# Kernel tuning notes

Hardware: AMD Instinct MI355X
Metric: run time of the kernel (lower is better)

## Reference

```python
import jax, jax.numpy as jnp
import numpy as np
import math

N, LQ, C = 4, 5440, 256
H, L, P = 8, 4, 4
D = C // H
SHAPES = [(64, 64), (32, 32), (16, 16), (8, 8)]
STARTS = [0, 4096, 5120, 5376]
LEN_IN = 5440


def setup_inputs() -> dict:
    key = jax.random.key(0)
    ks = jax.random.split(key, 12)
    s = 1.0 / math.sqrt(C)
    return {
        "query": jax.random.normal(ks[0], (N, LQ, C), jnp.float32),
        "reference_points": jax.random.uniform(ks[1], (N, LQ, L, 2), jnp.float32),
        "input_flatten": jax.random.normal(ks[2], (N, LEN_IN, C), jnp.float32),
        "input_spatial_shapes": jnp.asarray(SHAPES, jnp.int32),
        "input_level_start_index": jnp.asarray(STARTS, jnp.int32),
        "w_off": jax.random.normal(ks[3], (C, H * L * P * 2), jnp.float32) * 0.01,
        "b_off": jax.random.normal(ks[4], (H * L * P * 2,), jnp.float32) * 0.5,
        "w_attn": jax.random.normal(ks[5], (C, H * L * P), jnp.float32) * 0.01,
        "b_attn": jnp.zeros((H * L * P,), jnp.float32),
        "w_val": jax.random.normal(ks[6], (C, C), jnp.float32) * s,
        "b_val": jnp.zeros((C,), jnp.float32),
        "w_out": jax.random.normal(ks[7], (C, C), jnp.float32) * s,
        "b_out": jnp.zeros((C,), jnp.float32),
    }


def _gather_corner(lv, yi, xi, w):
    # lv: (N, h*w, H, D); yi, xi: (N, Lq, H, P) int32 -> (N, Lq, H, P, D)
    n, lq, h_, p_ = yi.shape
    idx = yi * w + xi
    idx2 = idx.transpose(0, 1, 3, 2).reshape(n, lq * p_, h_)[..., None]
    g = jnp.take_along_axis(lv, idx2, axis=1)  # (N, Lq*P, H, D)
    return g.reshape(n, lq, p_, h_, -1).transpose(0, 1, 3, 2, 4)


def _msdeform(query, reference_points, input_flatten, shapes, starts,
              w_off, b_off, w_attn, b_attn, w_val, b_val, w_out, b_out):
    n, lq, c = query.shape
    value = (input_flatten @ w_val + b_val).reshape(n, -1, H, D)
    off = (query @ w_off + b_off).reshape(n, lq, H, L, P, 2)
    attn = jax.nn.softmax((query @ w_attn + b_attn).reshape(n, lq, H, L * P), axis=-1)
    # sampling locations in [0,1], (N, Lq, H, L, P, 2)
    loc = jnp.clip(reference_points[:, :, None, :, None, :] + off, 0.0, 1.0)
    sampled = []
    for lvl, (hh, ww) in enumerate(shapes):
        s0 = starts[lvl]
        lv = value[:, s0:s0 + hh * ww]  # (N, hh*ww, H, D)
        xy = loc[:, :, :, lvl] * jnp.asarray([ww, hh], jnp.float32) - 0.5  # (N,Lq,H,P,2)
        x, y = xy[..., 0], xy[..., 1]
        x0 = jnp.floor(x)
        y0 = jnp.floor(y)
        x0i = jnp.clip(x0.astype(jnp.int32), 0, ww - 1)
        x1i = jnp.clip(x0.astype(jnp.int32) + 1, 0, ww - 1)
        y0i = jnp.clip(y0.astype(jnp.int32), 0, hh - 1)
        y1i = jnp.clip(y0.astype(jnp.int32) + 1, 0, hh - 1)
        x0f, x1f = x0i.astype(x.dtype), x1i.astype(x.dtype)
        y0f, y1f = y0i.astype(y.dtype), y1i.astype(y.dtype)
        wa = ((x1f - x) * (y1f - y))[..., None]
        wb = ((x1f - x) * (y - y0f))[..., None]
        wc = ((x - x0f) * (y1f - y))[..., None]
        wd = ((x - x0f) * (y - y0f))[..., None]
        va = _gather_corner(lv, y0i, x0i, ww)
        vb = _gather_corner(lv, y1i, x0i, ww)
        vc = _gather_corner(lv, y0i, x1i, ww)
        vd = _gather_corner(lv, y1i, x1i, ww)
        sampled.append(wa * va + wb * vb + wc * vc + wd * vd)
    sampled = jnp.concatenate(sampled, axis=3)  # (N, Lq, H, L*P, D)
    out = jnp.einsum('nqhp,nqhpd->nqhd', attn, sampled).reshape(n, lq, c)
    return out @ w_out + b_out


def reference(query, reference_points, input_flatten, input_spatial_shapes,
              input_level_start_index, w_off, b_off, w_attn, b_attn,
              w_val, b_val, w_out, b_out):
    shapes = [tuple(int(v) for v in row) for row in np.asarray(input_spatial_shapes)]
    starts = [int(v) for v in np.asarray(input_level_start_index)]
    return _msdeform(query, reference_points, input_flatten, shapes, starts,
                     w_off, b_off, w_attn, b_attn, w_val, b_val, w_out, b_out)
```

## Files before the change

### kernel.cpp

```cpp
#include <hip/hip_runtime.h>
#include <hip/hip_fp16.h>
#include <math.h>

#define C_DIM 256
#define H_DIM 8
#define L_DIM 4
#define P_DIM 4
#define LQ 5440
#define LEN_IN 5440
#define NB 4
#define M_ROWS (NB * LQ)

typedef __attribute__((ext_vector_type(8))) _Float16 f16x8;
typedef __attribute__((ext_vector_type(8))) unsigned short u16x8;
typedef __attribute__((ext_vector_type(4))) float f32x4;

__device__ __forceinline__ void split_f32(float a, __half& h, __half& l) {
    h = __float2half(a);
    l = __float2half(a - __half2float(h));
}

__global__ __launch_bounds__(256) void convert_wt(const float* __restrict__ w,
                                                  __half* __restrict__ hi,
                                                  __half* __restrict__ lo, int ncols) {
    const int ncol = blockIdx.x;
    const int k = threadIdx.x;
    const float a = w[(size_t)k * ncols + ncol];
    __half h, l;
    split_f32(a, h, l);
    hi[(size_t)ncol * 256 + k] = h;
    lo[(size_t)ncol * 256 + k] = l;
}

template <int NC>
__global__ __launch_bounds__(256, 2) void gemm_f16x3(const float* __restrict__ A,
                                                     const __half* __restrict__ Bhi,
                                                     const __half* __restrict__ Blo,
                                                     const float* __restrict__ bias,
                                                     float* __restrict__ outp) {
    __shared__ __align__(16) __half sA[2][128][32];
    __shared__ __align__(16) __half sB[2][128][32];

    const int n0 = blockIdx.x * 128;
    const int row0 = blockIdx.y * 128;
    const int t = threadIdx.x;
    const int w = t >> 6, lane = t & 63;
    const int bm = (w >> 1) * 64, bn = (w & 1) * 64;
    const int fr = lane & 15;
    const int fc = lane >> 4;

    const int ar1 = t >> 2, ar2 = ar1 + 64;
    const int ak8 = t & 3;
    const int asw1 = (ak8 ^ ((ar1 >> 1) & 3)) * 8;
    const int asw2 = (ak8 ^ ((ar2 >> 1) & 3)) * 8;
    const int br1 = t >> 2, br2 = br1 + 64;
    const int bc8 = t & 3;
    const int bsw1 = (bc8 ^ ((br1 >> 1) & 3)) * 8;
    const int bsw2 = (bc8 ^ ((br2 >> 1) & 3)) * 8;

    const size_t ga1 = (size_t)(row0 + ar1) * 256 + ak8 * 8;
    const size_t ga2 = (size_t)(row0 + ar2) * 256 + ak8 * 8;
    const size_t gb1 = (size_t)(n0 + br1) * 256 + bc8 * 8;
    const size_t gb2 = (size_t)(n0 + br2) * 256 + bc8 * 8;

    f32x4 acc[4][4];
#pragma unroll
    for (int m = 0; m < 4; ++m)
#pragma unroll
        for (int n = 0; n < 4; ++n)
#pragma unroll
            for (int r = 0; r < 4; ++r) acc[m][n][r] = 0.f;

    float4 pa[4];
    float4 pb[4];
    pa[0] = *(const float4*)(A + ga1);
    pa[1] = *(const float4*)(A + ga1 + 4);
    pa[2] = *(const float4*)(A + ga2);
    pa[3] = *(const float4*)(A + ga2 + 4);
    pb[0] = *(const float4*)(Bhi + gb1);
    pb[1] = *(const float4*)(Bhi + gb2);
    pb[2] = *(const float4*)(Blo + gb1);
    pb[3] = *(const float4*)(Blo + gb2);

    for (int kt = 0; kt < 8; ++kt) {
        if (kt) __syncthreads();
#pragma unroll
        for (int ch = 0; ch < 2; ++ch) {
            const float4 u = pa[2 * ch], v = pa[2 * ch + 1];
            const float e[8] = {u.x, u.y, u.z, u.w, v.x, v.y, v.z, v.w};
            u16x8 Hh, Ll;
#pragma unroll
            for (int i = 0; i < 8; ++i) {
                __half h, l;
                split_f32(e[i], h, l);
                Hh[i] = __half_as_ushort(h);
                Ll[i] = __half_as_ushort(l);
            }
            const int row = ch ? ar2 : ar1;
            const int sw = ch ? asw2 : asw1;
            *(u16x8*)&sA[0][row][sw] = Hh;
            *(u16x8*)&sA[1][row][sw] = Ll;
        }
        *(float4*)&sB[0][br1][bsw1] = pb[0];
        *(float4*)&sB[0][br2][bsw2] = pb[1];
        *(float4*)&sB[1][br1][bsw1] = pb[2];
        *(float4*)&sB[1][br2][bsw2] = pb[3];
        __syncthreads();
        if (kt < 7) {
            const size_t ko = (size_t)(kt + 1) * 32;
            pa[0] = *(const float4*)(A + ga1 + ko);
            pa[1] = *(const float4*)(A + ga1 + ko + 4);
            pa[2] = *(const float4*)(A + ga2 + ko);
            pa[3] = *(const float4*)(A + ga2 + ko + 4);
            pb[0] = *(const float4*)(Bhi + gb1 + ko);
            pb[1] = *(const float4*)(Bhi + gb2 + ko);
            pb[2] = *(const float4*)(Blo + gb1 + ko);
            pb[3] = *(const float4*)(Blo + gb2 + ko);
        }

        f16x8 bhf[4], blf[4];
#pragma unroll
        for (int n = 0; n < 4; ++n) {
            const int rowb = bn + n * 16 + fr;
            const int swb = (fc ^ ((rowb >> 1) & 3)) * 8;
            bhf[n] = *(const f16x8*)&sB[0][rowb][swb];
            blf[n] = *(const f16x8*)&sB[1][rowb][swb];
        }
#pragma unroll
        for (int m = 0; m < 4; ++m) {
            const int rowa = bm + m * 16 + fr;
            const int swa = (fc ^ ((rowa >> 1) & 3)) * 8;
            const f16x8 ah = *(const f16x8*)&sA[0][rowa][swa];
            const f16x8 al = *(const f16x8*)&sA[1][rowa][swa];
#pragma unroll
            for (int n = 0; n < 4; ++n) {
                acc[m][n] = __builtin_amdgcn_mfma_f32_16x16x32_f16(ah, bhf[n], acc[m][n], 0, 0, 0);
                acc[m][n] = __builtin_amdgcn_mfma_f32_16x16x32_f16(al, bhf[n], acc[m][n], 0, 0, 0);
                acc[m][n] = __builtin_amdgcn_mfma_f32_16x16x32_f16(ah, blf[n], acc[m][n], 0, 0, 0);
            }
        }
    }

#pragma unroll
    for (int n = 0; n < 4; ++n) {
        const int col = n0 + bn + n * 16 + fr;
        const float bv = bias[col];
#pragma unroll
        for (int m = 0; m < 4; ++m) {
            const int row = row0 + bm + m * 16 + fc * 4;
#pragma unroll
            for (int r = 0; r < 4; ++r)
                outp[(size_t)(row + r) * NC + col] = acc[m][n][r] + bv;
        }
    }
}

__global__ __launch_bounds__(128) void sample_kernel(const float* __restrict__ value,
                                                     const float* __restrict__ ol,
                                                     const float* __restrict__ refpts,
                                                     float* __restrict__ tmp) {
    const int t = threadIdx.x;
    const int w = t >> 6, lane = t & 63;
    const int q = blockIdx.x * 2 + w;
    const int n = q / LQ;

    __shared__ __align__(16) float4 s_aw[2][128];
    __shared__ __align__(16) int4 s_of[2][128];

#pragma unroll
    for (int s = 0; s < 2; ++s) {
        const int j = lane + 64 * s;
        const int h = j >> 4, lp = j & 15;
        const int l = lp >> 2;
        const int ww = 64 >> l;
        int st = 0;
        if (l == 1) st = 4096;
        else if (l == 2) st = 5120;
        else if (l == 3) st = 5376;

        const float2 oxy = *(const float2*)&ol[(size_t)q * 384 + 2 * j];
        const float2 rxy = *(const float2*)&refpts[((size_t)q * L_DIM + l) * 2];

        const float fw = (float)ww;
        const float x = fminf(fmaxf(rxy.x + oxy.x, 0.f), 1.f) * fw - 0.5f;
        const float y = fminf(fmaxf(rxy.y + oxy.y, 0.f), 1.f) * fw - 0.5f;
        const int xi = (int)floorf(x);
        const int yi = (int)floorf(y);
        const int x0i = min(max(xi, 0), ww - 1);
        const int x1i = min(max(xi + 1, 0), ww - 1);
        const int y0i = min(max(yi, 0), ww - 1);
        const int y1i = min(max(yi + 1, 0), ww - 1);
        const float wx0 = (float)x1i - x, wx1 = x - (float)x0i;
        const float wy0 = (float)y1i - y, wy1 = y - (float)y0i;

        const float lg = ol[(size_t)q * 384 + 256 + j];
        float m = lg;
#pragma unroll
        for (int o = 8; o; o >>= 1) m = fmaxf(m, __shfl_xor(m, o, 16));
        const float e = expf(lg - m);
        float sm = e;
#pragma unroll
        for (int o = 8; o; o >>= 1) sm += __shfl_xor(sm, o, 16);
        const float a = e / sm;

        const int p = lp * 8 + (h ^ (lp & 7));
        float4 aw;
        aw.x = a * (wx0 * wy0);
        aw.y = a * (wx0 * wy1);
        aw.z = a * (wx1 * wy0);
        aw.w = a * (wx1 * wy1);
        int4 of;
        of.x = (st + y0i * ww + x0i) << 10;
        of.y = (st + y1i * ww + x0i) << 10;
        of.z = (st + y0i * ww + x1i) << 10;
        of.w = (st + y1i * ww + x1i) << 10;
        s_aw[w][p] = aw;
        s_of[w][p] = of;
    }
    __syncthreads();

    const int h = lane >> 3;
    const char* vb = (const char*)value + (size_t)n * LEN_IN * C_DIM * 4 + (size_t)(lane * 16);
    float4 acc;
    acc.x = 0.f; acc.y = 0.f; acc.z = 0.f; acc.w = 0.f;
#pragma unroll
    for (int lp = 0; lp < 16; ++lp) {
        const int p = lp * 8 + (h ^ (lp & 7));
        const float4 aw = s_aw[w][p];
        const int4 of = s_of[w][p];
        const float4 v0 = *(const float4*)(vb + of.x);
        const float4 v1 = *(const float4*)(vb + of.y);
        const float4 v2 = *(const float4*)(vb + of.z);
        const float4 v3 = *(const float4*)(vb + of.w);
        acc.x += aw.x * v0.x + aw.y * v1.x + aw.z * v2.x + aw.w * v3.x;
        acc.y += aw.x * v0.y + aw.y * v1.y + aw.z * v2.y + aw.w * v3.y;
        acc.z += aw.x * v0.z + aw.y * v1.z + aw.z * v2.z + aw.w * v3.z;
        acc.w += aw.x * v0.w + aw.y * v1.w + aw.z * v2.w + aw.w * v3.w;
    }
    *(float4*)&tmp[(size_t)q * 256 + (size_t)(lane * 4)] = acc;
}

extern "C" void kernel_launch(void* const* d_in, const int* in_sizes, int n_in,
                              void* d_out, int out_size, void* d_ws, size_t ws_size,
                              hipStream_t stream) {
    const float* query         = (const float*)d_in[0];
    const float* refpts        = (const float*)d_in[1];
    const float* input_flatten = (const float*)d_in[2];
    const float* w_off  = (const float*)d_in[5];
    const float* b_off  = (const float*)d_in[6];
    const float* w_attn = (const float*)d_in[7];
    const float* b_attn = (const float*)d_in[8];
    const float* w_val  = (const float*)d_in[9];
    const float* b_val  = (const float*)d_in[10];
    const float* w_out  = (const float*)d_in[11];
    const float* b_out  = (const float*)d_in[12];
    float* out = (float*)d_out;

    const size_t nr = (size_t)M_ROWS;
    float* p = (float*)d_ws;
    float* value_ws = p; p += nr * 256;
    float* ol_ws    = p; p += nr * 384;
    float* tmp_ws   = p; p += nr * 256;
    float* bc_ws    = p; p += 384;
    __half* wv_hi = (__half*)p;
    __half* wv_lo = wv_hi + 256 * 256;
    __half* wc_hi = wv_lo + 256 * 256;
    __half* wc_lo = wc_hi + 384 * 256;
    __half* wt_hi = wc_lo + 384 * 256;
    __half* wt_lo = wt_hi + 256 * 256;

    convert_wt<<<256, 256, 0, stream>>>(w_val, wv_hi, wv_lo, 256);
    convert_wt<<<256, 256, 0, stream>>>(w_off, wc_hi, wc_lo, 256);
    convert_wt<<<128, 256, 0, stream>>>(w_attn, wc_hi + 256 * 256, wc_lo + 256 * 256, 128);
    convert_wt<<<256, 256, 0, stream>>>(w_out, wt_hi, wt_lo, 256);
    hipMemcpyAsync(bc_ws, b_off, 256 * sizeof(float), hipMemcpyDeviceToDevice, stream);
    hipMemcpyAsync(bc_ws + 256, b_attn, 128 * sizeof(float), hipMemcpyDeviceToDevice, stream);

    dim3 g256(2, M_ROWS / 128);
    dim3 g384(3, M_ROWS / 128);

    gemm_f16x3<256><<<g256, 256, 0, stream>>>(input_flatten, wv_hi, wv_lo, b_val, value_ws);
    gemm_f16x3<384><<<g384, 256, 0, stream>>>(query, wc_hi, wc_lo, bc_ws, ol_ws);

    sample_kernel<<<M_ROWS / 2, 128, 0, stream>>>(value_ws, ol_ws, refpts, tmp_ws);

    gemm_f16x3<256><<<g256, 256, 0, stream>>>(tmp_ws, wt_hi, wt_lo, b_out, out);
}
```

Measured before the change: 154.8 us.

## Merge weight conversions, narrow GEMM N-tile, and batch queries per sample block

Four weight-conversion launches and two bias memcpys become a single convert_all kernel to cut launch overhead. The GEMM is templated on N-tile width and min-waves, and the 256-column GEMMs now use 64-wide tiles with occupancy 3, giving more blocks and more resident waves. The sampling kernel moves to 256-thread blocks, each wave handling two queries in sequence, and uses unsigned offsets for address arithmetic. Narrower N tiles make each block reload the A operand more often, and fewer sample blocks could reduce latency hiding.

Measured after the change: 142.3 us. 1.09x faster.

```diff
diff --git a/kernel.cpp b/kernel.cpp
--- a/kernel.cpp
+++ b/kernel.cpp
@@ -20,32 +20,52 @@
     l = __float2half(a - __half2float(h));
 }
 
-__global__ __launch_bounds__(256) void convert_wt(const float* __restrict__ w,
-                                                  __half* __restrict__ hi,
-                                                  __half* __restrict__ lo, int ncols) {
-    const int ncol = blockIdx.x;
-    const int k = threadIdx.x;
-    const float a = w[(size_t)k * ncols + ncol];
-    __half h, l;
-    split_f32(a, h, l);
-    hi[(size_t)ncol * 256 + k] = h;
-    lo[(size_t)ncol * 256 + k] = l;
-}
-
-template <int NC>
-__global__ __launch_bounds__(256, 2) void gemm_f16x3(const float* __restrict__ A,
-                                                     const __half* __restrict__ Bhi,
-                                                     const __half* __restrict__ Blo,
-                                                     const float* __restrict__ bias,
-                                                     float* __restrict__ outp) {
+__global__ __launch_bounds__(256) void convert_all(const float* __restrict__ w_val,
+                                                   const float* __restrict__ w_off,
+                                                   const float* __restrict__ w_attn,
+                                                   const float* __restrict__ w_out,
+                                                   const float* __restrict__ b_off,
+                                                   const float* __restrict__ b_attn,
+                                                   __half* __restrict__ wv_hi, __half* __restrict__ wv_lo,
+                                                   __half* __restrict__ wc_hi, __half* __restrict__ wc_lo,
+                                                   __half* __restrict__ wt_hi, __half* __restrict__ wt_lo,
+                                                   float* __restrict__ bc) {
+    const int b = blockIdx.x, k = threadIdx.x;
+    if (b < 896) {
+        const float* w; __half *hi, *lo; int ncols, col, orow;
+        if (b < 256)      { w = w_val;  hi = wv_hi; lo = wv_lo; ncols = 256; col = b;       orow = col; }
+        else if (b < 512) { w = w_off;  hi = wc_hi; lo = wc_lo; ncols = 256; col = b - 256; orow = col; }
+        else if (b < 640) { w = w_attn; hi = wc_hi; lo = wc_lo; ncols = 128; col = b - 512; orow = col + 256; }
+        else              { w = w_out;  hi = wt_hi; lo = wt_lo; ncols = 256; col = b - 640; orow = col; }
+        const float a = w[(size_t)k * ncols + col];
+        __half h, l;
+        split_f32(a, h, l);
+        hi[(size_t)orow * 256 + k] = h;
+        lo[(size_t)orow * 256 + k] = l;
+    } else if (b == 896) {
+        bc[k] = b_off[k];
+    } else {
+        if (k < 128) bc[256 + k] = b_attn[k];
+    }
+}
+
+template <int NC, int BN, int MINW>
+__global__ __launch_bounds__(256, MINW) void gemm_f16x3(const float* __restrict__ A,
+                                                        const __half* __restrict__ Bhi,
+                                                        const __half* __restrict__ Blo,
+                                                        const float* __restrict__ bias,
+                                                        float* __restrict__ outp) {
+    constexpr int NF = BN / 32;
+    constexpr int BCH = BN / 64;
+
     __shared__ __align__(16) __half sA[2][128][32];
-    __shared__ __align__(16) __half sB[2][128][32];
-
-    const int n0 = blockIdx.x * 128;
+    __shared__ __align__(16) __half sB[2][BN][32];
+
+    const int n0 = blockIdx.x * BN;
     const int row0 = blockIdx.y * 128;
     const int t = threadIdx.x;
     const int w = t >> 6, lane = t & 63;
-    const int bm = (w >> 1) * 64, bn = (w & 1) * 64;
+    const int bm = (w >> 1) * 64, bn = (w & 1) * (BN / 2);
     const int fr = lane & 15;
     const int fc = lane >> 4;
 
@@ -53,34 +73,39 @@
     const int ak8 = t & 3;
     const int asw1 = (ak8 ^ ((ar1 >> 1) & 3)) * 8;
     const int asw2 = (ak8 ^ ((ar2 >> 1) & 3)) * 8;
-    const int br1 = t >> 2, br2 = br1 + 64;
     const int bc8 = t & 3;
-    const int bsw1 = (bc8 ^ ((br1 >> 1) & 3)) * 8;
-    const int bsw2 = (bc8 ^ ((br2 >> 1) & 3)) * 8;
+    int brr[BCH], bsw[BCH];
+#pragma unroll
+    for (int c = 0; c < BCH; ++c) {
+        brr[c] = (t >> 2) + 64 * c;
+        bsw[c] = (bc8 ^ ((brr[c] >> 1) & 3)) * 8;
+    }
 
     const size_t ga1 = (size_t)(row0 + ar1) * 256 + ak8 * 8;
     const size_t ga2 = (size_t)(row0 + ar2) * 256 + ak8 * 8;
-    const size_t gb1 = (size_t)(n0 + br1) * 256 + bc8 * 8;
-    const size_t gb2 = (size_t)(n0 + br2) * 256 + bc8 * 8;
-
-    f32x4 acc[4][4];
+    size_t gb[BCH];
+#pragma unroll
+    for (int c = 0; c < BCH; ++c) gb[c] = (size_t)(n0 + brr[c]) * 256 + bc8 * 8;
+
+    f32x4 acc[4][NF];
 #pragma unroll
     for (int m = 0; m < 4; ++m)
 #pragma unroll
-        for (int n = 0; n < 4; ++n)
+        for (int n = 0; n < NF; ++n)
 #pragma unroll
             for (int r = 0; r < 4; ++r) acc[m][n][r] = 0.f;
 
     float4 pa[4];
-    float4 pb[4];
+    float4 pb[2 * BCH];
     pa[0] = *(const float4*)(A + ga1);
     pa[1] = *(const float4*)(A + ga1 + 4);
     pa[2] = *(const float4*)(A + ga2);
     pa[3] = *(const float4*)(A + ga2 + 4);
-    pb[0] = *(const float4*)(Bhi + gb1);
-    pb[1] = *(const float4*)(Bhi + gb2);
-    pb[2] = *(const float4*)(Blo + gb1);
-    pb[3] = *(const float4*)(Blo + gb2);
+#pragma unroll
+    for (int c = 0; c < BCH; ++c) {
+        pb[c] = *(const float4*)(Bhi + gb[c]);
+        pb[BCH + c] = *(const float4*)(Blo + gb[c]);
+    }
 
     for (int kt = 0; kt < 8; ++kt) {
         if (kt) __syncthreads();
@@ -101,10 +126,11 @@
             *(u16x8*)&sA[0][row][sw] = Hh;
             *(u16x8*)&sA[1][row][sw] = Ll;
         }
-        *(float4*)&sB[0][br1][bsw1] = pb[0];
-        *(float4*)&sB[0][br2][bsw2] = pb[1];
-        *(float4*)&sB[1][br1][bsw1] = pb[2];
-        *(float4*)&sB[1][br2][bsw2] = pb[3];
+#pragma unroll
+        for (int c = 0; c < BCH; ++c) {
+            *(float4*)&sB[0][brr[c]][bsw[c]] = pb[c];
+            *(float4*)&sB[1][brr[c]][bsw[c]] = pb[BCH + c];
+        }
         __syncthreads();
         if (kt < 7) {
             const size_t ko = (size_t)(kt + 1) * 32;
@@ -112,15 +138,16 @@
             pa[1] = *(const float4*)(A + ga1 + ko + 4);
             pa[2] = *(const float4*)(A + ga2 + ko);
             pa[3] = *(const float4*)(A + ga2 + ko + 4);
-            pb[0] = *(const float4*)(Bhi + gb1 + ko);
-            pb[1] = *(const float4*)(Bhi + gb2 + ko);
-            pb[2] = *(const float4*)(Blo + gb1 + ko);
-            pb[3] = *(const float4*)(Blo + gb2 + ko);
-        }
-
-        f16x8 bhf[4], blf[4];
-#pragma unroll
-        for (int n = 0; n < 4; ++n) {
+#pragma unroll
+            for (int c = 0; c < BCH; ++c) {
+                pb[c] = *(const float4*)(Bhi + gb[c] + ko);
+                pb[BCH + c] = *(const float4*)(Blo + gb[c] + ko);
+            }
+        }
+
+        f16x8 bhf[NF], blf[NF];
+#pragma unroll
+        for (int n = 0; n < NF; ++n) {
             const int rowb = bn + n * 16 + fr;
             const int swb = (fc ^ ((rowb >> 1) & 3)) * 8;
             bhf[n] = *(const f16x8*)&sB[0][rowb][swb];
@@ -133,7 +160,7 @@
             const f16x8 ah = *(const f16x8*)&sA[0][rowa][swa];
             const f16x8 al = *(const f16x8*)&sA[1][rowa][swa];
 #pragma unroll
-            for (int n = 0; n < 4; ++n) {
+            for (int n = 0; n < NF; ++n) {
                 acc[m][n] = __builtin_amdgcn_mfma_f32_16x16x32_f16(ah, bhf[n], acc[m][n], 0, 0, 0);
                 acc[m][n] = __builtin_amdgcn_mfma_f32_16x16x32_f16(al, bhf[n], acc[m][n], 0, 0, 0);
                 acc[m][n] = __builtin_amdgcn_mfma_f32_16x16x32_f16(ah, blf[n], acc[m][n], 0, 0, 0);
@@ -142,7 +169,7 @@
     }
 
 #pragma unroll
-    for (int n = 0; n < 4; ++n) {
+    for (int n = 0; n < NF; ++n) {
         const int col = n0 + bn + n * 16 + fr;
         const float bv = bias[col];
 #pragma unroll
@@ -155,89 +182,93 @@
     }
 }
 
-__global__ __launch_bounds__(128) void sample_kernel(const float* __restrict__ value,
+__global__ __launch_bounds__(256) void sample_kernel(const float* __restrict__ value,
                                                      const float* __restrict__ ol,
                                                      const float* __restrict__ refpts,
                                                      float* __restrict__ tmp) {
     const int t = threadIdx.x;
     const int w = t >> 6, lane = t & 63;
-    const int q = blockIdx.x * 2 + w;
-    const int n = q / LQ;
-
-    __shared__ __align__(16) float4 s_aw[2][128];
-    __shared__ __align__(16) int4 s_of[2][128];
-
-#pragma unroll
-    for (int s = 0; s < 2; ++s) {
-        const int j = lane + 64 * s;
-        const int h = j >> 4, lp = j & 15;
-        const int l = lp >> 2;
-        const int ww = 64 >> l;
-        int st = 0;
-        if (l == 1) st = 4096;
-        else if (l == 2) st = 5120;
-        else if (l == 3) st = 5376;
-
-        const float2 oxy = *(const float2*)&ol[(size_t)q * 384 + 2 * j];
-        const float2 rxy = *(const float2*)&refpts[((size_t)q * L_DIM + l) * 2];
-
-        const float fw = (float)ww;
-        const float x = fminf(fmaxf(rxy.x + oxy.x, 0.f), 1.f) * fw - 0.5f;
-        const float y = fminf(fmaxf(rxy.y + oxy.y, 0.f), 1.f) * fw - 0.5f;
-        const int xi = (int)floorf(x);
-        const int yi = (int)floorf(y);
-        const int x0i = min(max(xi, 0), ww - 1);
-        const int x1i = min(max(xi + 1, 0), ww - 1);
-        const int y0i = min(max(yi, 0), ww - 1);
-        const int y1i = min(max(yi + 1, 0), ww - 1);
-        const float wx0 = (float)x1i - x, wx1 = x - (float)x0i;
-        const float wy0 = (float)y1i - y, wy1 = y - (float)y0i;
-
-        const float lg = ol[(size_t)q * 384 + 256 + j];
-        float m = lg;
-#pragma unroll
-        for (int o = 8; o; o >>= 1) m = fmaxf(m, __shfl_xor(m, o, 16));
-        const float e = expf(lg - m);
-        float sm = e;
-#pragma unroll
-        for (int o = 8; o; o >>= 1) sm += __shfl_xor(sm, o, 16);
-        const float a = e / sm;
-
-        const int p = lp * 8 + (h ^ (lp & 7));
-        float4 aw;
-        aw.x = a * (wx0 * wy0);
-        aw.y = a * (wx0 * wy1);
-        aw.z = a * (wx1 * wy0);
-        aw.w = a * (wx1 * wy1);
-        int4 of;
-        of.x = (st + y0i * ww + x0i) << 10;
-        of.y = (st + y1i * ww + x0i) << 10;
-        of.z = (st + y0i * ww + x1i) << 10;
-        of.w = (st + y1i * ww + x1i) << 10;
-        s_aw[w][p] = aw;
-        s_of[w][p] = of;
-    }
-    __syncthreads();
+
+    __shared__ __align__(16) float4 s_aw[4][128];
+    __shared__ __align__(16) uint4 s_of[4][128];
 
     const int h = lane >> 3;
-    const char* vb = (const char*)value + (size_t)n * LEN_IN * C_DIM * 4 + (size_t)(lane * 16);
-    float4 acc;
-    acc.x = 0.f; acc.y = 0.f; acc.z = 0.f; acc.w = 0.f;
-#pragma unroll
-    for (int lp = 0; lp < 16; ++lp) {
-        const int p = lp * 8 + (h ^ (lp & 7));
-        const float4 aw = s_aw[w][p];
-        const int4 of = s_of[w][p];
-        const float4 v0 = *(const float4*)(vb + of.x);
-        const float4 v1 = *(const float4*)(vb + of.y);
-        const float4 v2 = *(const float4*)(vb + of.z);
-        const float4 v3 = *(const float4*)(vb + of.w);
-        acc.x += aw.x * v0.x + aw.y * v1.x + aw.z * v2.x + aw.w * v3.x;
-        acc.y += aw.x * v0.y + aw.y * v1.y + aw.z * v2.y + aw.w * v3.y;
-        acc.z += aw.x * v0.z + aw.y * v1.z + aw.z * v2.z + aw.w * v3.z;
-        acc.w += aw.x * v0.w + aw.y * v1.w + aw.z * v2.w + aw.w * v3.w;
-    }
-    *(float4*)&tmp[(size_t)q * 256 + (size_t)(lane * 4)] = acc;
+    const unsigned l16 = (unsigned)(lane * 16);
+
+    for (int it = 0; it < 2; ++it) {
+        const int q = blockIdx.x * 8 + w * 2 + it;
+        const int n = q / LQ;
+
+#pragma unroll
+        for (int s = 0; s < 2; ++s) {
+            const int j = lane + 64 * s;
+            const int hq = j >> 4, lp = j & 15;
+            const int l = lp >> 2;
+            const int ww = 64 >> l;
+            int st = 0;
+            if (l == 1) st = 4096;
+            else if (l == 2) st = 5120;
+            else if (l == 3) st = 5376;
+
+            const float2 oxy = *(const float2*)&ol[(size_t)q * 384 + 2 * j];
+            const float2 rxy = *(const float2*)&refpts[((size_t)q * L_DIM + l) * 2];
+
+            const float fw = (float)ww;
+            const float x = fminf(fmaxf(rxy.x + oxy.x, 0.f), 1.f) * fw - 0.5f;
+            const float y = fminf(fmaxf(rxy.y + oxy.y, 0.f), 1.f) * fw - 0.5f;
+            const int xi = (int)floorf(x);
+            const int yi = (int)floorf(y);
+            const int x0i = min(max(xi, 0), ww - 1);
+            const int x1i = min(max(xi + 1, 0), ww - 1);
+            const int y0i = min(max(yi, 0), ww - 1);
+            const int y1i = min(max(yi + 1, 0), ww - 1);
+            const float wx0 = (float)x1i - x, wx1 = x - (float)x0i;
+            const float wy0 = (float)y1i - y, wy1 = y - (float)y0i;
+
+            const float lg = ol[(size_t)q * 384 + 256 + j];
+            float m = lg;
+#pragma unroll
+            for (int o = 8; o; o >>= 1) m = fmaxf(m, __shfl_xor(m, o, 16));
+            const float e = expf(lg - m);
+            float sm = e;
+#pragma unroll
+            for (int o = 8; o; o >>= 1) sm += __shfl_xor(sm, o, 16);
+            const float a = e / sm;
+
+            const int p = lp * 8 + (hq ^ (lp & 7));
+            float4 aw;
+            aw.x = a * (wx0 * wy0);
+            aw.y = a * (wx0 * wy1);
+            aw.z = a * (wx1 * wy0);
+            aw.w = a * (wx1 * wy1);
+            uint4 of;
+            of.x = (unsigned)(st + y0i * ww + x0i) << 10;
+            of.y = (unsigned)(st + y1i * ww + x0i) << 10;
+            of.z = (unsigned)(st + y0i * ww + x1i) << 10;
+            of.w = (unsigned)(st + y1i * ww + x1i) << 10;
+            s_aw[w][p] = aw;
+            s_of[w][p] = of;
+        }
+
+        const char* vbn = (const char*)value + (size_t)n * (LEN_IN * C_DIM * 4);
+        float4 acc;
+        acc.x = 0.f; acc.y = 0.f; acc.z = 0.f; acc.w = 0.f;
+#pragma unroll
+        for (int lp = 0; lp < 16; ++lp) {
+            const int p = lp * 8 + (h ^ (lp & 7));
+            const float4 aw = s_aw[w][p];
+            const uint4 of = s_of[w][p];
+            const float4 v0 = *(const float4*)(vbn + (of.x + l16));
+            const float4 v1 = *(const float4*)(vbn + (of.y + l16));
+            const float4 v2 = *(const float4*)(vbn + (of.z + l16));
+            const float4 v3 = *(const float4*)(vbn + (of.w + l16));
+            acc.x += aw.x * v0.x + aw.y * v1.x + aw.z * v2.x + aw.w * v3.x;
+            acc.y += aw.x * v0.y + aw.y * v1.y + aw.z * v2.y + aw.w * v3.y;
+            acc.z += aw.x * v0.z + aw.y * v1.z + aw.z * v2.z + aw.w * v3.z;
+            acc.w += aw.x * v0.w + aw.y * v1.w + aw.z * v2.w + aw.w * v3.w;
+        }
+        *(float4*)&tmp[(size_t)q * 256 + (size_t)(lane * 4)] = acc;
+    }
 }
 
 extern "C" void kernel_launch(void* const* d_in, const int* in_sizes, int n_in,
@@ -269,20 +300,16 @@
     __half* wt_hi = wc_lo + 384 * 256;
     __half* wt_lo = wt_hi + 256 * 256;
 
-    convert_wt<<<256, 256, 0, stream>>>(w_val, wv_hi, wv_lo, 256);
-    convert_wt<<<256, 256, 0, stream>>>(w_off, wc_hi, wc_lo, 256);
-    convert_wt<<<128, 256, 0, stream>>>(w_attn, wc_hi + 256 * 256, wc_lo + 256 * 256, 128);
-    convert_wt<<<256, 256, 0, stream>>>(w_out, wt_hi, wt_lo, 256);
-    hipMemcpyAsync(bc_ws, b_off, 256 * sizeof(float), hipMemcpyDeviceToDevice, stream);
-    hipMemcpyAsync(bc_ws + 256, b_attn, 128 * sizeof(float), hipMemcpyDeviceToDevice, stream);
-
-    dim3 g256(2, M_ROWS / 128);
+    convert_all<<<898, 256, 0, stream>>>(w_val, w_off, w_attn, w_out, b_off, b_attn,
+                                         wv_hi, wv_lo, wc_hi, wc_lo, wt_hi, wt_lo, bc_ws);
+
+    dim3 g256(4, M_ROWS / 128);
     dim3 g384(3, M_ROWS / 128);
 
-    gemm_f16x3<256><<<g256, 256, 0, stream>>>(input_flatten, wv_hi, wv_lo, b_val, value_ws);
-    gemm_f16x3<384><<<g384, 256, 0, stream>>>(query, wc_hi, wc_lo, bc_ws, ol_ws);
-
-    sample_kernel<<<M_ROWS / 2, 128, 0, stream>>>(value_ws, ol_ws, refpts, tmp_ws);
-
-    gemm_f16x3<256><<<g256, 256, 0, stream>>>(tmp_ws, wt_hi, wt_lo, b_out, out);
-}
+    gemm_f16x3<256, 64, 3><<<g256, 256, 0, stream>>>(input_flatten, wv_hi, wv_lo, b_val, value_ws);
+    gemm_f16x3<384, 128, 2><<<g384, 256, 0, stream>>>(query, wc_hi, wc_lo, bc_ws, ol_ws);
+
+    sample_kernel<<<M_ROWS / 8, 256, 0, stream>>>(value_ws, ol_ws, refpts, tmp_ws);
+
+    gemm_f16x3<256, 64, 3><<<g256, 256, 0, stream>>>(tmp_ws, wt_hi, wt_lo, b_out, out);
+}
```
